# Kernel optimization log

Hardware: AMD Instinct MI355X
Metric: run time of the kernel (lower is better)

## Reference

```python
import jax, jax.numpy as jnp
import numpy as np
from jax import lax

N_SAMPLES1 = 128   # self.n_samples[0]
K = 64             # k in sample_and_group
RADIUS = 0.4       # self.radius[0]
BN_EPS = 1e-5
NEG_INF = -1e8
DIMS0 = [6, 64, 64, 128]      # mlps_in[0][0] -> mlps[0]
DIMS1 = [131, 128, 128, 512]  # 128+3 -> mlps[1] (use_light_weight=False)


def _fps(pos, n):
    # pos: (N,3) -> (n,) indices; deterministic start at point 0
    Np = pos.shape[0]
    def body(carry, _):
        dists, last = carry
        d = jnp.sum((pos - pos[last]) ** 2, axis=-1)
        dists = jnp.minimum(dists, d)
        return (dists, jnp.argmax(dists).astype(jnp.int32)), last
    _, idxs = lax.scan(body, (jnp.full((Np,), 1e10, pos.dtype), jnp.int32(0)), None, length=n)
    return idxs


def _gather(values, idx):
    # values (B,N,C), idx (B,...) -> (B,...,C)
    return jax.vmap(lambda v, i: v[i])(values, idx)


def _conv_bn_relu(x, W, b, g, be):
    # 1x1 Conv2d + BatchNorm2d (training-mode batch stats) + ReLU; x (B,n,k,Cin)
    y = jnp.einsum('bnkc,cd->bnkd', x, W) + b
    m = jnp.mean(y, axis=(0, 1, 2), keepdims=True)
    v = jnp.mean(jnp.square(y - m), axis=(0, 1, 2), keepdims=True)
    return jax.nn.relu((y - m) * lax.rsqrt(v + BN_EPS) * g + be)


def _forward(x, pos,
             W00, b00, g00, be00, W01, b01, g01, be01, W02, b02, g02, be02,
             W10, b10, g10, be10, W11, b11, g11, be11, W12, b12, g12, be12):
    # ---- stage 0: FPS + kNN grouping + conv-MLP + radius-masked max pool ----
    fidx = jax.vmap(lambda p: _fps(p, N_SAMPLES1))(pos)          # (B,128)
    sp = _gather(pos, fidx)                                      # (B,128,3) sampled_pos
    # squared pairwise distances (||a||^2+||b||^2-2ab); topk/mask on sq dist is
    # equivalent to topk/mask on sqrt dist (monotone), avoids sqrt(0) NaN grads
    sq = (jnp.sum(sp ** 2, -1)[:, :, None] + jnp.sum(pos ** 2, -1)[:, None, :]
          - 2.0 * jnp.einsum('bmd,bnd->bmn', sp, pos))           # (B,128,N)
    sq = jnp.maximum(sq, 0.0)
    neg, tidx = lax.top_k(-sq, K)                                # smallest-k
    topk_sq = -neg                                               # (B,128,64)
    gp = _gather(pos, tidx) - sp[:, :, None, :]                  # centered grouped pos
    gf = jnp.concatenate([gp, _gather(x, tidx)], axis=-1)        # (B,128,64,6)
    for (W, b, g, be) in ((W00, b00, g00, be00), (W01, b01, g01, be01), (W02, b02, g02, be02)):
        gf = _conv_bn_relu(gf, W, b, g, be)                      # (B,128,64,128)
    mask = topk_sq <= RADIUS * RADIUS
    x1 = jnp.max(jnp.where(mask[..., None], gf, NEG_INF), axis=2)  # (B,128,128)
    # ---- stage 1: global (n_samples == 1) ----
    g2 = jnp.concatenate([sp, x1], axis=-1)[:, None]             # (B,1,128,131)
    for (W, b, g, be) in ((W10, b10, g10, be10), (W11, b11, g11, be11), (W12, b12, g12, be12)):
        g2 = _conv_bn_relu(g2, W, b, g, be)                      # (B,1,128,512)
    global_x = jnp.max(g2[:, 0], axis=1, keepdims=True)          # (B,1,512)
    return global_x


def setup_inputs() -> dict:
    key = jax.random.key(0)
    ks = jax.random.split(key, 16)
    B, N = 16, 8192
    inp = {
        'x': jax.random.normal(ks[0], (B, N, 3), jnp.float32),
        'pos': jax.random.uniform(ks[1], (B, N, 3), jnp.float32),
    }
    ki = 2
    for li, dims in enumerate([DIMS0, DIMS1]):
        for ci in range(3):
            cin, cout = dims[ci], dims[ci + 1]
            inp[f'W{li}{ci}'] = jax.random.normal(ks[ki], (cin, cout), jnp.float32) * 0.05
            inp[f'b{li}{ci}'] = jnp.zeros((cout,), jnp.float32)
            inp[f'g{li}{ci}'] = jnp.ones((cout,), jnp.float32)
            inp[f'be{li}{ci}'] = jnp.zeros((cout,), jnp.float32)
            ki += 1
    return inp


def reference(x, pos,
              W00, b00, g00, be00, W01, b01, g01, be01, W02, b02, g02, be02,
              W10, b10, g10, be10, W11, b11, g11, be11, W12, b12, g12, be12):
    global_x = _forward(x, pos,
                        W00, b00, g00, be00, W01, b01, g01, be01, W02, b02, g02, be02,
                        W10, b10, g10, be10, W11, b11, g11, be11, W12, b12, g12, be12)
    pos_out = jnp.zeros((pos.shape[0], 1, 3), pos.dtype)
    return global_x, pos_out
```

## Files before the change

### kernel.cpp

```cpp
#include <hip/hip_runtime.h>
#include <cstdint>
#include <cstddef>

#define NPTS 8192
#define BATCH 16
#define MS 128
#define KNB 64
#define NBLK (BATCH * MS)

__device__ __forceinline__ float dpp_wave_max_f32(float v) {
  v = fmaxf(v, __int_as_float(__builtin_amdgcn_update_dpp((int)0xff800000, __float_as_int(v), 0x111, 0xf, 0xf, false)));
  v = fmaxf(v, __int_as_float(__builtin_amdgcn_update_dpp((int)0xff800000, __float_as_int(v), 0x112, 0xf, 0xf, false)));
  v = fmaxf(v, __int_as_float(__builtin_amdgcn_update_dpp((int)0xff800000, __float_as_int(v), 0x114, 0xf, 0xf, false)));
  v = fmaxf(v, __int_as_float(__builtin_amdgcn_update_dpp((int)0xff800000, __float_as_int(v), 0x118, 0xf, 0xf, false)));
  v = fmaxf(v, __int_as_float(__builtin_amdgcn_update_dpp((int)0xff800000, __float_as_int(v), 0x142, 0xa, 0xf, false)));
  v = fmaxf(v, __int_as_float(__builtin_amdgcn_update_dpp((int)0xff800000, __float_as_int(v), 0x143, 0xc, 0xf, false)));
  return v;
}

__device__ __forceinline__ float dpp_wave_min_f32(float v) {
  v = fminf(v, __int_as_float(__builtin_amdgcn_update_dpp(0x7f800000, __float_as_int(v), 0x111, 0xf, 0xf, false)));
  v = fminf(v, __int_as_float(__builtin_amdgcn_update_dpp(0x7f800000, __float_as_int(v), 0x112, 0xf, 0xf, false)));
  v = fminf(v, __int_as_float(__builtin_amdgcn_update_dpp(0x7f800000, __float_as_int(v), 0x114, 0xf, 0xf, false)));
  v = fminf(v, __int_as_float(__builtin_amdgcn_update_dpp(0x7f800000, __float_as_int(v), 0x118, 0xf, 0xf, false)));
  v = fminf(v, __int_as_float(__builtin_amdgcn_update_dpp(0x7f800000, __float_as_int(v), 0x142, 0xa, 0xf, false)));
  v = fminf(v, __int_as_float(__builtin_amdgcn_update_dpp(0x7f800000, __float_as_int(v), 0x143, 0xc, 0xf, false)));
  return v;
}

__device__ __forceinline__ unsigned dpp_wave_min_u32(unsigned v) {
  unsigned o;
  o = (unsigned)__builtin_amdgcn_update_dpp((int)0xffffffffu, (int)v, 0x111, 0xf, 0xf, false); v = (o < v) ? o : v;
  o = (unsigned)__builtin_amdgcn_update_dpp((int)0xffffffffu, (int)v, 0x112, 0xf, 0xf, false); v = (o < v) ? o : v;
  o = (unsigned)__builtin_amdgcn_update_dpp((int)0xffffffffu, (int)v, 0x114, 0xf, 0xf, false); v = (o < v) ? o : v;
  o = (unsigned)__builtin_amdgcn_update_dpp((int)0xffffffffu, (int)v, 0x118, 0xf, 0xf, false); v = (o < v) ? o : v;
  o = (unsigned)__builtin_amdgcn_update_dpp((int)0xffffffffu, (int)v, 0x142, 0xa, 0xf, false); v = (o < v) ? o : v;
  o = (unsigned)__builtin_amdgcn_update_dpp((int)0xffffffffu, (int)v, 0x143, 0xc, 0xf, false); v = (o < v) ? o : v;
  return v;
}

__device__ __forceinline__ float dpp_row_max_f32(float v) {
  v = fmaxf(v, __int_as_float(__builtin_amdgcn_update_dpp((int)0xff800000, __float_as_int(v), 0x111, 0xf, 0xf, false)));
  v = fmaxf(v, __int_as_float(__builtin_amdgcn_update_dpp((int)0xff800000, __float_as_int(v), 0x112, 0xf, 0xf, false)));
  v = fmaxf(v, __int_as_float(__builtin_amdgcn_update_dpp((int)0xff800000, __float_as_int(v), 0x114, 0xf, 0xf, false)));
  v = fmaxf(v, __int_as_float(__builtin_amdgcn_update_dpp((int)0xff800000, __float_as_int(v), 0x118, 0xf, 0xf, false)));
  return v;
}

__device__ __forceinline__ unsigned dpp_row_min_u32(unsigned v) {
  unsigned o;
  o = (unsigned)__builtin_amdgcn_update_dpp((int)0xffffffffu, (int)v, 0x111, 0xf, 0xf, false); v = (o < v) ? o : v;
  o = (unsigned)__builtin_amdgcn_update_dpp((int)0xffffffffu, (int)v, 0x112, 0xf, 0xf, false); v = (o < v) ? o : v;
  o = (unsigned)__builtin_amdgcn_update_dpp((int)0xffffffffu, (int)v, 0x114, 0xf, 0xf, false); v = (o < v) ? o : v;
  o = (unsigned)__builtin_amdgcn_update_dpp((int)0xffffffffu, (int)v, 0x118, 0xf, 0xf, false); v = (o < v) ? o : v;
  return v;
}

__device__ __forceinline__ float dpp_quad_min_f32(float v) {
  v = fminf(v, __int_as_float(__builtin_amdgcn_update_dpp(0x7f800000, __float_as_int(v), 0x111, 0xf, 0xf, false)));
  v = fminf(v, __int_as_float(__builtin_amdgcn_update_dpp(0x7f800000, __float_as_int(v), 0x112, 0xf, 0xf, false)));
  return v;
}

__device__ __forceinline__ unsigned dpp_quad_min_u32(unsigned v) {
  unsigned o;
  o = (unsigned)__builtin_amdgcn_update_dpp((int)0xffffffffu, (int)v, 0x111, 0xf, 0xf, false); v = (o < v) ? o : v;
  o = (unsigned)__builtin_amdgcn_update_dpp((int)0xffffffffu, (int)v, 0x112, 0xf, 0xf, false); v = (o < v) ? o : v;
  return v;
}

#define FPS_STEP(J)                                                        \
  {                                                                        \
    const float4 p = pts4[J * 1024 + t];                                   \
    const float dx = p.x - lx;                                             \
    const float dy = p.y - ly;                                             \
    const float dz = p.z - lz;                                             \
    const float d = dx * dx + dy * dy + dz * dz;                           \
    md##J = fminf(md##J, d);                                               \
  }

#define FPS_RESCAN(J)                                                      \
  if (md##J == wv) best = (unsigned)(J * 1024 + t);

__global__ __launch_bounds__(1024, 4) void fps_kernel(const float* __restrict__ pos,
                                                      float* __restrict__ sp) {
#pragma clang fp contract(off)
  extern __shared__ float4 pts4[];
  __shared__ float wval[2][16];
  __shared__ unsigned widx[2][16];
  const int b = blockIdx.x;
  const float* P = pos + (size_t)b * NPTS * 3;
  const int t = threadIdx.x;
  const int wave = t >> 6;
  const int lane = t & 63;
  float md0 = 1e10f, md1 = 1e10f, md2 = 1e10f, md3 = 1e10f;
  float md4 = 1e10f, md5 = 1e10f, md6 = 1e10f, md7 = 1e10f;
  for (int i = t; i < NPTS; i += 1024)
    pts4[i] = make_float4(P[i * 3 + 0], P[i * 3 + 1], P[i * 3 + 2], 0.f);
  float lx = P[0], ly = P[1], lz = P[2];
  __syncthreads();
  for (int it = 0; it < MS; ++it) {
    if (t == 0) {
      sp[((size_t)b * MS + it) * 3 + 0] = lx;
      sp[((size_t)b * MS + it) * 3 + 1] = ly;
      sp[((size_t)b * MS + it) * 3 + 2] = lz;
    }
    FPS_STEP(0) FPS_STEP(1) FPS_STEP(2) FPS_STEP(3)
    FPS_STEP(4) FPS_STEP(5) FPS_STEP(6) FPS_STEP(7)
    const float m01 = fmaxf(md0, md1), m23 = fmaxf(md2, md3);
    const float m45 = fmaxf(md4, md5), m67 = fmaxf(md6, md7);
    const float bv = fmaxf(fmaxf(m01, m23), fmaxf(m45, m67));
    const float wv = __int_as_float(
        __builtin_amdgcn_readlane(__float_as_int(dpp_wave_max_f32(bv)), 63));
    unsigned best = 0xffffffffu;
    if (bv == wv) {
      FPS_RESCAN(7) FPS_RESCAN(6) FPS_RESCAN(5) FPS_RESCAN(4)
      FPS_RESCAN(3) FPS_RESCAN(2) FPS_RESCAN(1) FPS_RESCAN(0)
    }
    const unsigned wi =
        (unsigned)__builtin_amdgcn_readlane((int)dpp_wave_min_u32(best), 63);
    const int par = it & 1;
    if (lane == 0) { wval[par][wave] = wv; widx[par][wave] = wi; }
    __syncthreads();
    const float a = wval[par][lane & 15];
    const float M = __int_as_float(
        __builtin_amdgcn_readlane(__float_as_int(dpp_row_max_f32(a)), 15));
    const unsigned c2 = (a == M) ? widx[par][lane & 15] : 0xffffffffu;
    const unsigned idx =
        (unsigned)__builtin_amdgcn_readlane((int)dpp_row_min_u32(c2), 15);
    const float4 c = pts4[idx];
    lx = c.x; ly = c.y; lz = c.z;
  }
}

__global__ __launch_bounds__(256) void knn_kernel(const float* __restrict__ pos,
                                                  const float* __restrict__ xf,
                                                  const float* __restrict__ sp,
                                                  float* __restrict__ gf0,
                                                  float* __restrict__ sqsel) {
#pragma clang fp contract(off)
  __shared__ float sqv[NPTS];
  __shared__ float wval[2][4];
  __shared__ unsigned widx[2][4];
  __shared__ int sel_i[KNB];
  __shared__ float sel_v[KNB];
  const int bm = blockIdx.x;
  const int b = bm >> 7;
  const float* P = pos + (size_t)b * NPTS * 3;
  const float sx = sp[bm * 3 + 0], sy = sp[bm * 3 + 1], sz = sp[bm * 3 + 2];
  const float nsp = sx * sx + sy * sy + sz * sz;
  const int t = threadIdx.x;
  const int wave = t >> 6;
  const int lane = t & 63;
  for (int j = 0; j < 32; ++j) {
    const int i = j * 256 + t;
    const float qx = P[i * 3 + 0], qy = P[i * 3 + 1], qz = P[i * 3 + 2];
    const float npos = qx * qx + qy * qy + qz * qz;
    const float dt = sx * qx + sy * qy + sz * qz;
    float sq = (nsp + npos) - 2.0f * dt;
    sq = fmaxf(sq, 0.0f);
    sqv[i] = sq;
  }
  __syncthreads();
  float cv;
  unsigned ci;
  {
    unsigned long long k0 = ~0ULL;
    for (int j = 0; j < 32; ++j) {
      const int i = j * 256 + t;
      const unsigned long long key =
          ((unsigned long long)__float_as_uint(sqv[i]) << 32) | (unsigned)i;
      if (key < k0) k0 = key;
    }
    cv = __uint_as_float((unsigned)(k0 >> 32));
    ci = (unsigned)k0;
  }
  for (int round = 0; round < KNB; ++round) {
    const float wv = __int_as_float(
        __builtin_amdgcn_readlane(__float_as_int(dpp_wave_min_f32(cv)), 63));
    const unsigned sel = (cv == wv) ? ci : 0xffffffffu;
    const unsigned wi =
        (unsigned)__builtin_amdgcn_readlane((int)dpp_wave_min_u32(sel), 63);
    const int par = round & 1;
    if (lane == 0) { wval[par][wave] = wv; widx[par][wave] = wi; }
    __syncthreads();
    const float a = wval[par][lane & 3];
    const float M = __int_as_float(
        __builtin_amdgcn_readlane(__float_as_int(dpp_quad_min_f32(a)), 3));
    const unsigned c2 = (a == M) ? widx[par][lane & 3] : 0xffffffffu;
    const unsigned idx =
        (unsigned)__builtin_amdgcn_readlane((int)dpp_quad_min_u32(c2), 3);
    const int col = (int)(idx & 255u);
    if (t == col) {
      sel_i[round] = (int)idx;
      sel_v[round] = M;
      sqv[idx] = __uint_as_float(0x7f800000u);
    }
    if (wave == (col >> 6)) {
      float v = __uint_as_float(0x7f800000u);
      unsigned ii = 0xffffffffu;
      if (lane < 32) {
        const int i = lane * 256 + col;
        v = sqv[i];
        if (i == (int)idx) v = __uint_as_float(0x7f800000u);
        ii = (unsigned)i;
      }
      const float mv = __int_as_float(
          __builtin_amdgcn_readlane(__float_as_int(dpp_wave_min_f32(v)), 63));
      const unsigned s2 = (v == mv) ? ii : 0xffffffffu;
      const unsigned mi =
          (unsigned)__builtin_amdgcn_readlane((int)dpp_wave_min_u32(s2), 63);
      if (t == col) { cv = mv; ci = mi; }
    }
  }
  __syncthreads();
  if (t < KNB) {
    const int i = sel_i[t];
    const float* X = xf + (size_t)b * NPTS * 3;
    const size_t base = ((size_t)bm * KNB + t) * 6;
    gf0[base + 0] = P[i * 3 + 0] - sx;
    gf0[base + 1] = P[i * 3 + 1] - sy;
    gf0[base + 2] = P[i * 3 + 2] - sz;
    gf0[base + 3] = X[i * 3 + 0];
    gf0[base + 4] = X[i * 3 + 1];
    gf0[base + 5] = X[i * 3 + 2];
    sqsel[(size_t)bm * KNB + t] = sel_v[t];
  }
}


__global__ __launch_bounds__(256) void l1_kernel(
    const float* __restrict__ gf0, const float* __restrict__ W0,
    const float* __restrict__ B0,
    float* __restrict__ psum, float* __restrict__ psq,
    float* __restrict__ y1pre) {
  __shared__ float in6[64 * 8];
  __shared__ float wbuf[384];
  __shared__ float out[64 * 65];
  const int blk = blockIdx.x;
  const int t = threadIdx.x;
  const float* G = gf0 + (size_t)blk * 384;
  for (int i = t; i < 384; i += 256) in6[(i / 6) * 8 + (i % 6)] = G[i];
  for (int i = t; i < 384; i += 256) wbuf[i] = W0[i];
  __syncthreads();
  const int r = t >> 2;
  const int c0 = (t & 3) * 16;
  float acc[16];
#pragma unroll
  for (int j = 0; j < 16; ++j) acc[j] = B0[c0 + j];
  for (int cin = 0; cin < 6; ++cin) {
    const float a = in6[r * 8 + cin];
#pragma unroll
    for (int j = 0; j < 16; ++j) acc[j] = fmaf(a, wbuf[cin * 64 + c0 + j], acc[j]);
  }
#pragma unroll
  for (int j = 0; j < 16; ++j) out[r * 65 + c0 + j] = acc[j];
  __syncthreads();
  if (t < 64) {
    float s = 0.f, q = 0.f;
    for (int r2 = 0; r2 < 64; ++r2) { const float v = out[r2 * 65 + t]; s += v; q += v * v; }
    psum[(size_t)t * NBLK + blk] = s;
    psq[(size_t)t * NBLK + blk] = q;
  }
  float* Y = y1pre + (size_t)blk * 4096;
  for (int i = t; i < 4096; i += 256) Y[i] = out[(i >> 6) * 65 + (i & 63)];
}

__global__ __launch_bounds__(256) void l2_kernel(
    const float* __restrict__ ypre, const float* __restrict__ sc,
    const float* __restrict__ sh, const float* __restrict__ W1,
    const float* __restrict__ B1,
    float* __restrict__ psum, float* __restrict__ psq,
    float* __restrict__ yout) {
  __shared__ float As[64 * 68];
  __shared__ float Bs[64 * 64];
  __shared__ float out[64 * 68];
  const int blk = blockIdx.x;
  const int t = threadIdx.x;
  const float* Y = ypre + (size_t)blk * 4096;
  for (int i = t; i < 4096; i += 256) {
    const int c = i & 63;
    As[(i >> 6) * 68 + c] = fmaxf(fmaf(Y[i], sc[c], sh[c]), 0.f);
  }
  for (int i = t; i < 4096; i += 256) Bs[i] = W1[i];
  __syncthreads();
  const int tr = t >> 4;
  const int tc4 = (t & 15) * 4;
  float acc[4][4];
#pragma unroll
  for (int s = 0; s < 4; ++s)
#pragma unroll
    for (int j = 0; j < 4; ++j) acc[s][j] = B1[tc4 + j];
  for (int k0 = 0; k0 < 64; k0 += 4) {
    float4 av[4];
#pragma unroll
    for (int s = 0; s < 4; ++s)
      av[s] = *reinterpret_cast<const float4*>(&As[(tr + 16 * s) * 68 + k0]);
#pragma unroll
    for (int kk = 0; kk < 4; ++kk) {
      const float4 bv = *reinterpret_cast<const float4*>(&Bs[(k0 + kk) * 64 + tc4]);
#pragma unroll
      for (int s = 0; s < 4; ++s) {
        const float a = (kk == 0) ? av[s].x : (kk == 1) ? av[s].y
                       : (kk == 2) ? av[s].z : av[s].w;
        acc[s][0] = fmaf(a, bv.x, acc[s][0]);
        acc[s][1] = fmaf(a, bv.y, acc[s][1]);
        acc[s][2] = fmaf(a, bv.z, acc[s][2]);
        acc[s][3] = fmaf(a, bv.w, acc[s][3]);
      }
    }
  }
#pragma unroll
  for (int s = 0; s < 4; ++s) {
    float4 o;
    o.x = acc[s][0]; o.y = acc[s][1]; o.z = acc[s][2]; o.w = acc[s][3];
    *reinterpret_cast<float4*>(&out[(tr + 16 * s) * 68 + tc4]) = o;
  }
  __syncthreads();
  if (t < 64) {
    float s = 0.f, q = 0.f;
    for (int r2 = 0; r2 < 64; ++r2) { const float v = out[r2 * 68 + t]; s += v; q += v * v; }
    psum[(size_t)t * NBLK + blk] = s;
    psq[(size_t)t * NBLK + blk] = q;
  }
  float* O = yout + (size_t)blk * 4096;
  for (int i = t; i < 4096; i += 256) O[i] = out[(i >> 6) * 68 + (i & 63)];
}

__global__ __launch_bounds__(256) void l3_kernel(
    const float* __restrict__ ypre, const float* __restrict__ sc,
    const float* __restrict__ sh, const float* __restrict__ W2,
    const float* __restrict__ B2,
    float* __restrict__ psum, float* __restrict__ psq,
    float* __restrict__ yout) {
  __shared__ float As[64 * 68];
  __shared__ float Bs[64 * 64];
  __shared__ float out[64 * 68];
  const int blk = blockIdx.x;
  const int t = threadIdx.x;
  const float* Y = ypre + (size_t)blk * 4096;
  for (int i = t; i < 4096; i += 256) {
    const int c = i & 63;
    As[(i >> 6) * 68 + c] = fmaxf(fmaf(Y[i], sc[c], sh[c]), 0.f);
  }
  const int tr = t >> 4;
  const int tc4 = (t & 15) * 4;
  for (int hc = 0; hc < 2; ++hc) {
    __syncthreads();
    for (int i = t; i < 4096; i += 256)
      Bs[i] = W2[(i >> 6) * 128 + hc * 64 + (i & 63)];
    __syncthreads();
    float acc[4][4];
#pragma unroll
    for (int s = 0; s < 4; ++s)
#pragma unroll
      for (int j = 0; j < 4; ++j) acc[s][j] = B2[hc * 64 + tc4 + j];
    for (int k0 = 0; k0 < 64; k0 += 4) {
      float4 av[4];
#pragma unroll
      for (int s = 0; s < 4; ++s)
        av[s] = *reinterpret_cast<const float4*>(&As[(tr + 16 * s) * 68 + k0]);
#pragma unroll
      for (int kk = 0; kk < 4; ++kk) {
        const float4 bv = *reinterpret_cast<const float4*>(&Bs[(k0 + kk) * 64 + tc4]);
#pragma unroll
        for (int s = 0; s < 4; ++s) {
          const float a = (kk == 0) ? av[s].x : (kk == 1) ? av[s].y
                         : (kk == 2) ? av[s].z : av[s].w;
          acc[s][0] = fmaf(a, bv.x, acc[s][0]);
          acc[s][1] = fmaf(a, bv.y, acc[s][1]);
          acc[s][2] = fmaf(a, bv.z, acc[s][2]);
          acc[s][3] = fmaf(a, bv.w, acc[s][3]);
        }
      }
    }
#pragma unroll
    for (int s = 0; s < 4; ++s) {
      float4 o;
      o.x = acc[s][0]; o.y = acc[s][1]; o.z = acc[s][2]; o.w = acc[s][3];
      *reinterpret_cast<float4*>(&out[(tr + 16 * s) * 68 + tc4]) = o;
    }
    __syncthreads();
    if (t < 64) {
      float s = 0.f, q = 0.f;
      for (int r2 = 0; r2 < 64; ++r2) { const float v = out[r2 * 68 + t]; s += v; q += v * v; }
      psum[(size_t)(hc * 64 + t) * NBLK + blk] = s;
      psq[(size_t)(hc * 64 + t) * NBLK + blk] = q;
    }
    float* O = yout + (size_t)blk * 8192;
    for (int i = t; i < 4096; i += 256)
      O[(i >> 6) * 128 + hc * 64 + (i & 63)] = out[(i >> 6) * 68 + (i & 63)];
  }
}

__global__ __launch_bounds__(128) void l4_kernel(
    const float* __restrict__ y3pre, const float* __restrict__ sc3,
    const float* __restrict__ sh3, const float* __restrict__ sqsel,
    float* __restrict__ x1) {
  __shared__ float sqs[64];
  const int blk = blockIdx.x;
  const int t = threadIdx.x;
  if (t < 64) sqs[t] = sqsel[(size_t)blk * 64 + t];
  __syncthreads();
  const float scv = sc3[t], shv = sh3[t];
  const float* Y = y3pre + (size_t)blk * 8192;
  float mx = -1e8f;
  for (int r = 0; r < 64; ++r) {
    const float act = fmaxf(fmaf(Y[r * 128 + t], scv, shv), 0.f);
    const float v = (sqs[r] <= 0.16f) ? act : -1e8f;
    mx = fmaxf(mx, v);
  }
  x1[(size_t)blk * 128 + t] = mx;
}

template <int MODE>
__global__ __launch_bounds__(256) void chain_kernel(
    const float* __restrict__ gf0,
    const float* __restrict__ W0, const float* __restrict__ B0,
    const float* __restrict__ W1, const float* __restrict__ B1,
    const float* __restrict__ W2, const float* __restrict__ B2,
    const float* __restrict__ sc1, const float* __restrict__ sh1,
    const float* __restrict__ sc2, const float* __restrict__ sh2,
    const float* __restrict__ sc3, const float* __restrict__ sh3,
    const float* __restrict__ sqsel,
    float* __restrict__ psum, float* __restrict__ psq, float* __restrict__ x1) {
  __shared__ float tA[64 * 65];
  __shared__ float tB[64 * 65];
  __shared__ float wbuf[64 * 64];
  __shared__ float in6[64 * 8];
  __shared__ float sqs[64];
  const int blk = blockIdx.x;
  const int t = threadIdx.x;
  {
    const float* G = gf0 + (size_t)blk * 64 * 6;
    for (int i = t; i < 384; i += 256) in6[(i / 6) * 8 + (i % 6)] = G[i];
    for (int i = t; i < 384; i += 256) wbuf[i] = W0[i];
    if (MODE == 4 && t < 64) sqs[t] = sqsel[(size_t)blk * 64 + t];
  }
  __syncthreads();
  const int r = t >> 2;
  const int c0 = (t & 3) * 16;
  float acc[16];
#pragma unroll
  for (int j = 0; j < 16; ++j) acc[j] = B0[c0 + j];
  for (int cin = 0; cin < 6; ++cin) {
    const float a = in6[r * 8 + cin];
#pragma unroll
    for (int j = 0; j < 16; ++j) acc[j] = fmaf(a, wbuf[cin * 64 + c0 + j], acc[j]);
  }
  if (MODE == 1) {
#pragma unroll
    for (int j = 0; j < 16; ++j) tA[r * 65 + c0 + j] = acc[j];
    __syncthreads();
    if (t < 64) {
      float s = 0.f, q = 0.f;
      for (int r2 = 0; r2 < 64; ++r2) { const float v = tA[r2 * 65 + t]; s += v; q += v * v; }
      psum[(size_t)t * NBLK + blk] = s;
      psq[(size_t)t * NBLK + blk] = q;
    }
    return;
  }
#pragma unroll
  for (int j = 0; j < 16; ++j) {
    const int c = c0 + j;
    tA[r * 65 + c] = fmaxf(fmaf(acc[j], sc1[c], sh1[c]), 0.f);
  }
  __syncthreads();
  for (int i = t; i < 4096; i += 256) wbuf[i] = W1[i];
  __syncthreads();
#pragma unroll
  for (int j = 0; j < 16; ++j) acc[j] = B1[c0 + j];
  for (int cin = 0; cin < 64; ++cin) {
    const float a = tA[r * 65 + cin];
    const float4* w4 = reinterpret_cast<const float4*>(&wbuf[cin * 64 + c0]);
#pragma unroll
    for (int k = 0; k < 4; ++k) {
      const float4 w = w4[k];
      acc[k * 4 + 0] = fmaf(a, w.x, acc[k * 4 + 0]);
      acc[k * 4 + 1] = fmaf(a, w.y, acc[k * 4 + 1]);
      acc[k * 4 + 2] = fmaf(a, w.z, acc[k * 4 + 2]);
      acc[k * 4 + 3] = fmaf(a, w.w, acc[k * 4 + 3]);
    }
  }
  if (MODE == 2) {
#pragma unroll
    for (int j = 0; j < 16; ++j) tB[r * 65 + c0 + j] = acc[j];
    __syncthreads();
    if (t < 64) {
      float s = 0.f, q = 0.f;
      for (int r2 = 0; r2 < 64; ++r2) { const float v = tB[r2 * 65 + t]; s += v; q += v * v; }
      psum[(size_t)t * NBLK + blk] = s;
      psq[(size_t)t * NBLK + blk] = q;
    }
    return;
  }
#pragma unroll
  for (int j = 0; j < 16; ++j) {
    const int c = c0 + j;
    tB[r * 65 + c] = fmaxf(fmaf(acc[j], sc2[c], sh2[c]), 0.f);
  }
  for (int hc = 0; hc < 2; ++hc) {
    __syncthreads();
    for (int i = t; i < 4096; i += 256) {
      const int cin = i >> 6, cc = i & 63;
      wbuf[i] = W2[cin * 128 + hc * 64 + cc];
    }
    __syncthreads();
    float st_s = 0.f, st_q = 0.f, mx = -1e8f;
    for (int rh = 0; rh < 2; ++rh) {
      const int rr = rh * 32 + (t >> 3);
      const int cc0 = (t & 7) * 8;
      float a3[8];
#pragma unroll
      for (int j = 0; j < 8; ++j) a3[j] = B2[hc * 64 + cc0 + j];
      for (int cin = 0; cin < 64; ++cin) {
        const float a = tB[rr * 65 + cin];
        const float4* w4 = reinterpret_cast<const float4*>(&wbuf[cin * 64 + cc0]);
#pragma unroll
        for (int k = 0; k < 2; ++k) {
          const float4 w = w4[k];
          a3[k * 4 + 0] = fmaf(a, w.x, a3[k * 4 + 0]);
          a3[k * 4 + 1] = fmaf(a, w.y, a3[k * 4 + 1]);
          a3[k * 4 + 2] = fmaf(a, w.z, a3[k * 4 + 2]);
          a3[k * 4 + 3] = fmaf(a, w.w, a3[k * 4 + 3]);
        }
      }
      __syncthreads();
#pragma unroll
      for (int j = 0; j < 8; ++j) tA[(t >> 3) * 65 + cc0 + j] = a3[j];
      __syncthreads();
      if (t < 64) {
        if (MODE == 3) {
          for (int q2 = 0; q2 < 32; ++q2) { const float v = tA[q2 * 65 + t]; st_s += v; st_q += v * v; }
        } else {
          const float scv = sc3[hc * 64 + t], shv = sh3[hc * 64 + t];
          for (int q2 = 0; q2 < 32; ++q2) {
            const int kidx = rh * 32 + q2;
            const float y = tA[q2 * 65 + t];
            const float act = fmaxf(fmaf(y, scv, shv), 0.f);
            const float v = (sqs[kidx] <= 0.16f) ? act : -1e8f;
            mx = fmaxf(mx, v);
          }
        }
      }
      __syncthreads();
    }
    if (t < 64) {
      if (MODE == 3) {
        psum[(size_t)(hc * 64 + t) * NBLK + blk] = st_s;
        psq[(size_t)(hc * 64 + t) * NBLK + blk] = st_q;
      } else if (MODE == 4) {
        x1[(size_t)blk * 128 + hc * 64 + t] = mx;
      }
    }
  }
}

__global__ __launch_bounds__(256) void p_stats(const float* __restrict__ psum,
                                               const float* __restrict__ psq,
                                               float invN,
                                               const float* __restrict__ g,
                                               const float* __restrict__ be,
                                               float* __restrict__ sc,
                                               float* __restrict__ sh) {
  const int c = blockIdx.x;
  const int t = threadIdx.x;
  double s = 0.0, q = 0.0;
  for (int k = t; k < NBLK; k += 256) {
    s += (double)psum[(size_t)c * NBLK + k];
    q += (double)psq[(size_t)c * NBLK + k];
  }
  __shared__ double ss[256], qq[256];
  ss[t] = s;
  qq[t] = q;
  __syncthreads();
  for (int st = 128; st > 0; st >>= 1) {
    if (t < st) { ss[t] += ss[t + st]; qq[t] += qq[t + st]; }
    __syncthreads();
  }
  if (t == 0) {
    const double mean = ss[0] * (double)invN;
    double var = qq[0] * (double)invN - mean * mean;
    if (var < 0.0) var = 0.0;
    const float scl = (float)((double)g[c] / sqrt(var + 1e-5));
    sc[c] = scl;
    sh[c] = be[c] - (float)mean * scl;
  }
}

__global__ __launch_bounds__(128) void s1_kernel(const float* __restrict__ sp,
                                                 const float* __restrict__ x1,
                                                 const float* __restrict__ W,
                                                 const float* __restrict__ bia,
                                                 float* __restrict__ y1) {
  __shared__ float row[132];
  const int rowid = blockIdx.x;
  const int t = threadIdx.x;
  if (t < 3) row[t] = sp[(size_t)rowid * 3 + t];
  row[3 + t] = x1[(size_t)rowid * 128 + t];
  __syncthreads();
  float acc = bia[t];
  for (int cin = 0; cin < 131; ++cin) acc = fmaf(row[cin], W[(size_t)cin * 128 + t], acc);
  y1[(size_t)rowid * 128 + t] = acc;
}

__global__ __launch_bounds__(128) void s2_kernel(const float* __restrict__ y1,
                                                 const float* __restrict__ sc, const float* __restrict__ sh,
                                                 const float* __restrict__ W, const float* __restrict__ bia,
                                                 float* __restrict__ y2) {
  __shared__ float row[128];
  const int rowid = blockIdx.x;
  const int t = threadIdx.x;
  row[t] = fmaxf(fmaf(y1[(size_t)rowid * 128 + t], sc[t], sh[t]), 0.f);
  __syncthreads();
  float acc = bia[t];
  for (int cin = 0; cin < 128; ++cin) acc = fmaf(row[cin], W[(size_t)cin * 128 + t], acc);
  y2[(size_t)rowid * 128 + t] = acc;
}

__global__ __launch_bounds__(256) void s3_kernel(const float* __restrict__ y2,
                                                 const float* __restrict__ sc, const float* __restrict__ sh,
                                                 const float* __restrict__ W, const float* __restrict__ bia,
                                                 float* __restrict__ y3) {
  __shared__ float row[128];
  const int rowid = blockIdx.x;
  const int t = threadIdx.x;
  if (t < 128) row[t] = fmaxf(fmaf(y2[(size_t)rowid * 128 + t], sc[t], sh[t]), 0.f);
  __syncthreads();
  for (int h = 0; h < 2; ++h) {
    const int c = h * 256 + t;
    float acc = bia[c];
    for (int cin = 0; cin < 128; ++cin) acc = fmaf(row[cin], W[(size_t)cin * 512 + c], acc);
    y3[(size_t)rowid * 512 + c] = acc;
  }
}

__global__ __launch_bounds__(256) void s_stats(const float* __restrict__ y, int C, int rows,
                                               const float* __restrict__ g, const float* __restrict__ be,
                                               float* __restrict__ sc, float* __restrict__ sh) {
  const int c = blockIdx.x;
  const int t = threadIdx.x;
  double s = 0.0, q = 0.0;
  for (int r2 = t; r2 < rows; r2 += 256) {
    const double v = (double)y[(size_t)r2 * C + c];
    s += v;
    q += v * v;
  }
  __shared__ double ss[256], qq[256];
  ss[t] = s;
  qq[t] = q;
  __syncthreads();
  for (int st = 128; st > 0; st >>= 1) {
    if (t < st) { ss[t] += ss[t + st]; qq[t] += qq[t + st]; }
    __syncthreads();
  }
  if (t == 0) {
    const double mean = ss[0] / rows;
    double var = qq[0] / rows - mean * mean;
    if (var < 0.0) var = 0.0;
    const float scl = (float)((double)g[c] / sqrt(var + 1e-5));
    sc[c] = scl;
    sh[c] = be[c] - (float)mean * scl;
  }
}

__global__ __launch_bounds__(256) void final_kernel(const float* __restrict__ y3,
                                                    const float* __restrict__ sc, const float* __restrict__ sh,
                                                    float* __restrict__ out) {
  const int gid = blockIdx.x * 256 + threadIdx.x;
  const int b = gid >> 9;
  const int c = gid & 511;
  const float scv = sc[c], shv = sh[c];
  float mx = -3.402823466e+38f;
  for (int m = 0; m < 128; ++m) {
    const float v = fmaxf(fmaf(y3[((size_t)(b * 128 + m)) * 512 + c], scv, shv), 0.f);
    mx = fmaxf(mx, v);
  }
  out[gid] = mx;
  if (gid < 48) out[8192 + gid] = 0.f;
}

extern "C" void kernel_launch(void* const* d_in, const int* in_sizes, int n_in,
                              void* d_out, int out_size, void* d_ws, size_t ws_size,
                              hipStream_t stream) {
  const float* x    = (const float*)d_in[0];
  const float* pos  = (const float*)d_in[1];
  const float* W00  = (const float*)d_in[2];
  const float* b00  = (const float*)d_in[3];
  const float* g00  = (const float*)d_in[4];
  const float* be00 = (const float*)d_in[5];
  const float* W01  = (const float*)d_in[6];
  const float* b01  = (const float*)d_in[7];
  const float* g01  = (const float*)d_in[8];
  const float* be01 = (const float*)d_in[9];
  const float* W02  = (const float*)d_in[10];
  const float* b02  = (const float*)d_in[11];
  const float* g02  = (const float*)d_in[12];
  const float* be02 = (const float*)d_in[13];
  const float* W10  = (const float*)d_in[14];
  const float* b10  = (const float*)d_in[15];
  const float* g10  = (const float*)d_in[16];
  const float* be10 = (const float*)d_in[17];
  const float* W11  = (const float*)d_in[18];
  const float* b11  = (const float*)d_in[19];
  const float* g11  = (const float*)d_in[20];
  const float* be11 = (const float*)d_in[21];
  const float* W12  = (const float*)d_in[22];
  const float* b12  = (const float*)d_in[23];
  const float* g12  = (const float*)d_in[24];
  const float* be12 = (const float*)d_in[25];

  float* w = (float*)d_ws;
  float* sp    = w;
  float* gf0   = sp + 6144;
  float* sqsel = gf0 + 786432;
  float* x1    = sqsel + 131072;
  float* parts = x1 + 262144;
  float* psum  = parts;
  float* psq   = parts + 128 * NBLK;
  float* st    = parts + 524288;
  float* sc1 = st + 0,    *sh1 = st + 64;
  float* sc2 = st + 128,  *sh2 = st + 192;
  float* sc3 = st + 256,  *sh3 = st + 384;
  float* t1sc = st + 512, *t1sh = st + 640;
  float* t2sc = st + 768, *t2sh = st + 896;
  float* t3sc = st + 1024, *t3sh = st + 1536;
  float* y1s = st + 2048;
  float* y2s = y1s + 262144;
  float* y3s = y2s + 262144;
  const size_t BASE = 3284992;
  float* y1pre = w + BASE;
  float* y2pre = y1pre + 8388608;
  float* y3pre = y2pre + 8388608;
  const size_t NEED = BASE + 8388608ULL * 2 + 16777216ULL;
  const bool big = ws_size >= NEED * sizeof(float);

  fps_kernel<<<BATCH, 1024, NPTS * sizeof(float4), stream>>>(pos, sp);
  knn_kernel<<<BATCH * MS, 256, 0, stream>>>(pos, x, sp, gf0, sqsel);

  const float invN0 = 1.0f / (float)(NBLK * KNB);
  if (big) {
    l1_kernel<<<NBLK, 256, 0, stream>>>(gf0, W00, b00, psum, psq, y1pre);
    p_stats<<<64, 256, 0, stream>>>(psum, psq, invN0, g00, be00, sc1, sh1);
    l2_kernel<<<NBLK, 256, 0, stream>>>(y1pre, sc1, sh1, W01, b01, psum, psq, y2pre);
    p_stats<<<64, 256, 0, stream>>>(psum, psq, invN0, g01, be01, sc2, sh2);
    l3_kernel<<<NBLK, 256, 0, stream>>>(y2pre, sc2, sh2, W02, b02, psum, psq, y3pre);
    p_stats<<<128, 256, 0, stream>>>(psum, psq, invN0, g02, be02, sc3, sh3);
    l4_kernel<<<NBLK, 128, 0, stream>>>(y3pre, sc3, sh3, sqsel, x1);
  } else {
    chain_kernel<1><<<NBLK, 256, 0, stream>>>(gf0, W00, b00, W01, b01, W02, b02,
                                              sc1, sh1, sc2, sh2, sc3, sh3, sqsel, psum, psq, x1);
    p_stats<<<64, 256, 0, stream>>>(psum, psq, invN0, g00, be00, sc1, sh1);
    chain_kernel<2><<<NBLK, 256, 0, stream>>>(gf0, W00, b00, W01, b01, W02, b02,
                                              sc1, sh1, sc2, sh2, sc3, sh3, sqsel, psum, psq, x1);
    p_stats<<<64, 256, 0, stream>>>(psum, psq, invN0, g01, be01, sc2, sh2);
    chain_kernel<3><<<NBLK, 256, 0, stream>>>(gf0, W00, b00, W01, b01, W02, b02,
                                              sc1, sh1, sc2, sh2, sc3, sh3, sqsel, psum, psq, x1);
    p_stats<<<128, 256, 0, stream>>>(psum, psq, invN0, g02, be02, sc3, sh3);
    chain_kernel<4><<<NBLK, 256, 0, stream>>>(gf0, W00, b00, W01, b01, W02, b02,
                                              sc1, sh1, sc2, sh2, sc3, sh3, sqsel, psum, psq, x1);
  }

  s1_kernel<<<NBLK, 128, 0, stream>>>(sp, x1, W10, b10, y1s);
  s_stats<<<128, 256, 0, stream>>>(y1s, 128, NBLK, g10, be10, t1sc, t1sh);
  s2_kernel<<<NBLK, 128, 0, stream>>>(y1s, t1sc, t1sh, W11, b11, y2s);
  s_stats<<<128, 256, 0, stream>>>(y2s, 128, NBLK, g11, be11, t2sc, t2sh);
  s3_kernel<<<NBLK, 256, 0, stream>>>(y2s, t2sc, t2sh, W12, b12, y3s);
  s_stats<<<512, 256, 0, stream>>>(y3s, 512, NBLK, g12, be12, t3sc, t3sh);
  final_kernel<<<32, 256, 0, stream>>>(y3s, t3sc, t3sh, (float*)d_out);
}
```

Measured before the change: 440.5 us.

## Make kNN top-k selection per-wave without block barriers, then merge lists

The kNN kernel now has each of its four waves pick its own 64 smallest candidates without a block-wide barrier per round. It tracks already-taken entries with a per-column bitmask rather than writing infinity into shared memory, and pads the shared distance array to avoid bank conflicts. The four sorted per-wave lists are then merged by binary-search ranking to get the global top 64. Distance computation is fused into the initial min scan, and the unused chain_kernel fallback is removed so the big-workspace path is always taken. This risks failing if the workspace is smaller than required.

After: 432.2 us. No clear change (-1.9%).

```diff
diff --git a/kernel.cpp b/kernel.cpp
--- a/kernel.cpp
+++ b/kernel.cpp
@@ -53,19 +53,6 @@
   o = (unsigned)__builtin_amdgcn_update_dpp((int)0xffffffffu, (int)v, 0x112, 0xf, 0xf, false); v = (o < v) ? o : v;
   o = (unsigned)__builtin_amdgcn_update_dpp((int)0xffffffffu, (int)v, 0x114, 0xf, 0xf, false); v = (o < v) ? o : v;
   o = (unsigned)__builtin_amdgcn_update_dpp((int)0xffffffffu, (int)v, 0x118, 0xf, 0xf, false); v = (o < v) ? o : v;
-  return v;
-}
-
-__device__ __forceinline__ float dpp_quad_min_f32(float v) {
-  v = fminf(v, __int_as_float(__builtin_amdgcn_update_dpp(0x7f800000, __float_as_int(v), 0x111, 0xf, 0xf, false)));
-  v = fminf(v, __int_as_float(__builtin_amdgcn_update_dpp(0x7f800000, __float_as_int(v), 0x112, 0xf, 0xf, false)));
-  return v;
-}
-
-__device__ __forceinline__ unsigned dpp_quad_min_u32(unsigned v) {
-  unsigned o;
-  o = (unsigned)__builtin_amdgcn_update_dpp((int)0xffffffffu, (int)v, 0x111, 0xf, 0xf, false); v = (o < v) ? o : v;
-  o = (unsigned)__builtin_amdgcn_update_dpp((int)0xffffffffu, (int)v, 0x112, 0xf, 0xf, false); v = (o < v) ? o : v;
   return v;
 }
 
@@ -139,11 +126,9 @@
                                                   float* __restrict__ gf0,
                                                   float* __restrict__ sqsel) {
 #pragma clang fp contract(off)
-  __shared__ float sqv[NPTS];
-  __shared__ float wval[2][4];
-  __shared__ unsigned widx[2][4];
-  __shared__ int sel_i[KNB];
-  __shared__ float sel_v[KNB];
+  __shared__ float sqv[NPTS + 32];
+  __shared__ unsigned long long wlist[4][KNB];
+  __shared__ unsigned long long selk[KNB];
   const int bm = blockIdx.x;
   const int b = bm >> 7;
   const float* P = pos + (size_t)b * NPTS * 3;
@@ -152,70 +137,76 @@
   const int t = threadIdx.x;
   const int wave = t >> 6;
   const int lane = t & 63;
-  for (int j = 0; j < 32; ++j) {
-    const int i = j * 256 + t;
-    const float qx = P[i * 3 + 0], qy = P[i * 3 + 1], qz = P[i * 3 + 2];
-    const float npos = qx * qx + qy * qy + qz * qz;
-    const float dt = sx * qx + sy * qy + sz * qz;
-    float sq = (nsp + npos) - 2.0f * dt;
-    sq = fmaxf(sq, 0.0f);
-    sqv[i] = sq;
-  }
-  __syncthreads();
   float cv;
   unsigned ci;
   {
     unsigned long long k0 = ~0ULL;
     for (int j = 0; j < 32; ++j) {
       const int i = j * 256 + t;
+      const float qx = P[i * 3 + 0], qy = P[i * 3 + 1], qz = P[i * 3 + 2];
+      const float npos = qx * qx + qy * qy + qz * qz;
+      const float dt = sx * qx + sy * qy + sz * qz;
+      float sq = (nsp + npos) - 2.0f * dt;
+      sq = fmaxf(sq, 0.0f);
+      sqv[i + j] = sq;
       const unsigned long long key =
-          ((unsigned long long)__float_as_uint(sqv[i]) << 32) | (unsigned)i;
+          ((unsigned long long)__float_as_uint(sq) << 32) | (unsigned)i;
       if (key < k0) k0 = key;
     }
     cv = __uint_as_float((unsigned)(k0 >> 32));
     ci = (unsigned)k0;
   }
+  __syncthreads();
+  unsigned cmask = 0u;
   for (int round = 0; round < KNB; ++round) {
     const float wv = __int_as_float(
         __builtin_amdgcn_readlane(__float_as_int(dpp_wave_min_f32(cv)), 63));
     const unsigned sel = (cv == wv) ? ci : 0xffffffffu;
     const unsigned wi =
         (unsigned)__builtin_amdgcn_readlane((int)dpp_wave_min_u32(sel), 63);
-    const int par = round & 1;
-    if (lane == 0) { wval[par][wave] = wv; widx[par][wave] = wi; }
-    __syncthreads();
-    const float a = wval[par][lane & 3];
-    const float M = __int_as_float(
-        __builtin_amdgcn_readlane(__float_as_int(dpp_quad_min_f32(a)), 3));
-    const unsigned c2 = (a == M) ? widx[par][lane & 3] : 0xffffffffu;
-    const unsigned idx =
-        (unsigned)__builtin_amdgcn_readlane((int)dpp_quad_min_u32(c2), 3);
-    const int col = (int)(idx & 255u);
-    if (t == col) {
-      sel_i[round] = (int)idx;
-      sel_v[round] = M;
-      sqv[idx] = __uint_as_float(0x7f800000u);
-    }
-    if (wave == (col >> 6)) {
-      float v = __uint_as_float(0x7f800000u);
-      unsigned ii = 0xffffffffu;
-      if (lane < 32) {
-        const int i = lane * 256 + col;
-        v = sqv[i];
-        if (i == (int)idx) v = __uint_as_float(0x7f800000u);
-        ii = (unsigned)i;
-      }
-      const float mv = __int_as_float(
-          __builtin_amdgcn_readlane(__float_as_int(dpp_wave_min_f32(v)), 63));
-      const unsigned s2 = (v == mv) ? ii : 0xffffffffu;
-      const unsigned mi =
-          (unsigned)__builtin_amdgcn_readlane((int)dpp_wave_min_u32(s2), 63);
-      if (t == col) { cv = mv; ci = mi; }
-    }
+    if (lane == 0)
+      wlist[wave][round] =
+          ((unsigned long long)__float_as_uint(wv) << 32) | wi;
+    const int col = (int)(wi & 255u);
+    const int ownerLane = col & 63;
+    const unsigned jsel = wi >> 8;
+    if (lane == ownerLane) cmask |= (1u << jsel);
+    const unsigned omask =
+        (unsigned)__builtin_amdgcn_readlane((int)cmask, ownerLane);
+    float v = __uint_as_float(0x7f800000u);
+    unsigned ii = 0xffffffffu;
+    if (lane < 32 && !((omask >> lane) & 1u)) {
+      const int i = lane * 256 + col;
+      v = sqv[i + lane];
+      ii = (unsigned)i;
+    }
+    const float mv = __int_as_float(
+        __builtin_amdgcn_readlane(__float_as_int(dpp_wave_min_f32(v)), 63));
+    const unsigned s2 = (v == mv) ? ii : 0xffffffffu;
+    const unsigned mi =
+        (unsigned)__builtin_amdgcn_readlane((int)dpp_wave_min_u32(s2), 63);
+    if (lane == ownerLane) { cv = mv; ci = mi; }
+  }
+  __syncthreads();
+  {
+    const int w = wave, r = lane;
+    const unsigned long long e = wlist[w][r];
+    int rank = r;
+#pragma unroll
+    for (int w2 = 0; w2 < 4; ++w2) {
+      if (w2 == w) continue;
+      int lo = 0;
+#pragma unroll
+      for (int step = 32; step > 0; step >>= 1)
+        if (lo + step <= KNB && wlist[w2][lo + step - 1] < e) lo += step;
+      rank += lo;
+    }
+    if (rank < KNB) selk[rank] = e;
   }
   __syncthreads();
   if (t < KNB) {
-    const int i = sel_i[t];
+    const unsigned long long e = selk[t];
+    const int i = (int)(e & 0xffffffffu);
     const float* X = xf + (size_t)b * NPTS * 3;
     const size_t base = ((size_t)bm * KNB + t) * 6;
     gf0[base + 0] = P[i * 3 + 0] - sx;
@@ -224,7 +215,7 @@
     gf0[base + 3] = X[i * 3 + 0];
     gf0[base + 4] = X[i * 3 + 1];
     gf0[base + 5] = X[i * 3 + 2];
-    sqsel[(size_t)bm * KNB + t] = sel_v[t];
+    sqsel[(size_t)bm * KNB + t] = __uint_as_float((unsigned)(e >> 32));
   }
 }
 
@@ -411,149 +402,6 @@
     mx = fmaxf(mx, v);
   }
   x1[(size_t)blk * 128 + t] = mx;
-}
-
-template <int MODE>
-__global__ __launch_bounds__(256) void chain_kernel(
-    const float* __restrict__ gf0,
-    const float* __restrict__ W0, const float* __restrict__ B0,
-    const float* __restrict__ W1, const float* __restrict__ B1,
-    const float* __restrict__ W2, const float* __restrict__ B2,
-    const float* __restrict__ sc1, const float* __restrict__ sh1,
-    const float* __restrict__ sc2, const float* __restrict__ sh2,
-    const float* __restrict__ sc3, const float* __restrict__ sh3,
-    const float* __restrict__ sqsel,
-    float* __restrict__ psum, float* __restrict__ psq, float* __restrict__ x1) {
-  __shared__ float tA[64 * 65];
-  __shared__ float tB[64 * 65];
-  __shared__ float wbuf[64 * 64];
-  __shared__ float in6[64 * 8];
-  __shared__ float sqs[64];
-  const int blk = blockIdx.x;
-  const int t = threadIdx.x;
-  {
-    const float* G = gf0 + (size_t)blk * 64 * 6;
-    for (int i = t; i < 384; i += 256) in6[(i / 6) * 8 + (i % 6)] = G[i];
-    for (int i = t; i < 384; i += 256) wbuf[i] = W0[i];
-    if (MODE == 4 && t < 64) sqs[t] = sqsel[(size_t)blk * 64 + t];
-  }
-  __syncthreads();
-  const int r = t >> 2;
-  const int c0 = (t & 3) * 16;
-  float acc[16];
-#pragma unroll
-  for (int j = 0; j < 16; ++j) acc[j] = B0[c0 + j];
-  for (int cin = 0; cin < 6; ++cin) {
-    const float a = in6[r * 8 + cin];
-#pragma unroll
-    for (int j = 0; j < 16; ++j) acc[j] = fmaf(a, wbuf[cin * 64 + c0 + j], acc[j]);
-  }
-  if (MODE == 1) {
-#pragma unroll
-    for (int j = 0; j < 16; ++j) tA[r * 65 + c0 + j] = acc[j];
-    __syncthreads();
-    if (t < 64) {
-      float s = 0.f, q = 0.f;
-      for (int r2 = 0; r2 < 64; ++r2) { const float v = tA[r2 * 65 + t]; s += v; q += v * v; }
-      psum[(size_t)t * NBLK + blk] = s;
-      psq[(size_t)t * NBLK + blk] = q;
-    }
-    return;
-  }
-#pragma unroll
-  for (int j = 0; j < 16; ++j) {
-    const int c = c0 + j;
-    tA[r * 65 + c] = fmaxf(fmaf(acc[j], sc1[c], sh1[c]), 0.f);
-  }
-  __syncthreads();
-  for (int i = t; i < 4096; i += 256) wbuf[i] = W1[i];
-  __syncthreads();
-#pragma unroll
-  for (int j = 0; j < 16; ++j) acc[j] = B1[c0 + j];
-  for (int cin = 0; cin < 64; ++cin) {
-    const float a = tA[r * 65 + cin];
-    const float4* w4 = reinterpret_cast<const float4*>(&wbuf[cin * 64 + c0]);
-#pragma unroll
-    for (int k = 0; k < 4; ++k) {
-      const float4 w = w4[k];
-      acc[k * 4 + 0] = fmaf(a, w.x, acc[k * 4 + 0]);
-      acc[k * 4 + 1] = fmaf(a, w.y, acc[k * 4 + 1]);
-      acc[k * 4 + 2] = fmaf(a, w.z, acc[k * 4 + 2]);
-      acc[k * 4 + 3] = fmaf(a, w.w, acc[k * 4 + 3]);
-    }
-  }
-  if (MODE == 2) {
-#pragma unroll
-    for (int j = 0; j < 16; ++j) tB[r * 65 + c0 + j] = acc[j];
-    __syncthreads();
-    if (t < 64) {
-      float s = 0.f, q = 0.f;
-      for (int r2 = 0; r2 < 64; ++r2) { const float v = tB[r2 * 65 + t]; s += v; q += v * v; }
-      psum[(size_t)t * NBLK + blk] = s;
-      psq[(size_t)t * NBLK + blk] = q;
-    }
-    return;
-  }
-#pragma unroll
-  for (int j = 0; j < 16; ++j) {
-    const int c = c0 + j;
-    tB[r * 65 + c] = fmaxf(fmaf(acc[j], sc2[c], sh2[c]), 0.f);
-  }
-  for (int hc = 0; hc < 2; ++hc) {
-    __syncthreads();
-    for (int i = t; i < 4096; i += 256) {
-      const int cin = i >> 6, cc = i & 63;
-      wbuf[i] = W2[cin * 128 + hc * 64 + cc];
-    }
-    __syncthreads();
-    float st_s = 0.f, st_q = 0.f, mx = -1e8f;
-    for (int rh = 0; rh < 2; ++rh) {
-      const int rr = rh * 32 + (t >> 3);
-      const int cc0 = (t & 7) * 8;
-      float a3[8];
-#pragma unroll
-      for (int j = 0; j < 8; ++j) a3[j] = B2[hc * 64 + cc0 + j];
-      for (int cin = 0; cin < 64; ++cin) {
-        const float a = tB[rr * 65 + cin];
-        const float4* w4 = reinterpret_cast<const float4*>(&wbuf[cin * 64 + cc0]);
-#pragma unroll
-        for (int k = 0; k < 2; ++k) {
-          const float4 w = w4[k];
-          a3[k * 4 + 0] = fmaf(a, w.x, a3[k * 4 + 0]);
-          a3[k * 4 + 1] = fmaf(a, w.y, a3[k * 4 + 1]);
-          a3[k * 4 + 2] = fmaf(a, w.z, a3[k * 4 + 2]);
-          a3[k * 4 + 3] = fmaf(a, w.w, a3[k * 4 + 3]);
-        }
-      }
-      __syncthreads();
-#pragma unroll
-      for (int j = 0; j < 8; ++j) tA[(t >> 3) * 65 + cc0 + j] = a3[j];
-      __syncthreads();
-      if (t < 64) {
-        if (MODE == 3) {
-          for (int q2 = 0; q2 < 32; ++q2) { const float v = tA[q2 * 65 + t]; st_s += v; st_q += v * v; }
-        } else {
-          const float scv = sc3[hc * 64 + t], shv = sh3[hc * 64 + t];
-          for (int q2 = 0; q2 < 32; ++q2) {
-            const int kidx = rh * 32 + q2;
-            const float y = tA[q2 * 65 + t];
-            const float act = fmaxf(fmaf(y, scv, shv), 0.f);
-            const float v = (sqs[kidx] <= 0.16f) ? act : -1e8f;
-            mx = fmaxf(mx, v);
-          }
-        }
-      }
-      __syncthreads();
-    }
-    if (t < 64) {
-      if (MODE == 3) {
-        psum[(size_t)(hc * 64 + t) * NBLK + blk] = st_s;
-        psq[(size_t)(hc * 64 + t) * NBLK + blk] = st_q;
-      } else if (MODE == 4) {
-        x1[(size_t)blk * 128 + hc * 64 + t] = mx;
-      }
-    }
-  }
 }
 
 __global__ __launch_bounds__(256) void p_stats(const float* __restrict__ psum,
@@ -733,33 +581,19 @@
   float* y2pre = y1pre + 8388608;
   float* y3pre = y2pre + 8388608;
   const size_t NEED = BASE + 8388608ULL * 2 + 16777216ULL;
-  const bool big = ws_size >= NEED * sizeof(float);
+  (void)NEED;
 
   fps_kernel<<<BATCH, 1024, NPTS * sizeof(float4), stream>>>(pos, sp);
   knn_kernel<<<BATCH * MS, 256, 0, stream>>>(pos, x, sp, gf0, sqsel);
 
   const float invN0 = 1.0f / (float)(NBLK * KNB);
-  if (big) {
-    l1_kernel<<<NBLK, 256, 0, stream>>>(gf0, W00, b00, psum, psq, y1pre);
-    p_stats<<<64, 256, 0, stream>>>(psum, psq, invN0, g00, be00, sc1, sh1);
-    l2_kernel<<<NBLK, 256, 0, stream>>>(y1pre, sc1, sh1, W01, b01, psum, psq, y2pre);
-    p_stats<<<64, 256, 0, stream>>>(psum, psq, invN0, g01, be01, sc2, sh2);
-    l3_kernel<<<NBLK, 256, 0, stream>>>(y2pre, sc2, sh2, W02, b02, psum, psq, y3pre);
-    p_stats<<<128, 256, 0, stream>>>(psum, psq, invN0, g02, be02, sc3, sh3);
-    l4_kernel<<<NBLK, 128, 0, stream>>>(y3pre, sc3, sh3, sqsel, x1);
-  } else {
-    chain_kernel<1><<<NBLK, 256, 0, stream>>>(gf0, W00, b00, W01, b01, W02, b02,
-                                              sc1, sh1, sc2, sh2, sc3, sh3, sqsel, psum, psq, x1);
-    p_stats<<<64, 256, 0, stream>>>(psum, psq, invN0, g00, be00, sc1, sh1);
-    chain_kernel<2><<<NBLK, 256, 0, stream>>>(gf0, W00, b00, W01, b01, W02, b02,
-                                              sc1, sh1, sc2, sh2, sc3, sh3, sqsel, psum, psq, x1);
-    p_stats<<<64, 256, 0, stream>>>(psum, psq, invN0, g01, be01, sc2, sh2);
-    chain_kernel<3><<<NBLK, 256, 0, stream>>>(gf0, W00, b00, W01, b01, W02, b02,
-                                              sc1, sh1, sc2, sh2, sc3, sh3, sqsel, psum, psq, x1);
-    p_stats<<<128, 256, 0, stream>>>(psum, psq, invN0, g02, be02, sc3, sh3);
-    chain_kernel<4><<<NBLK, 256, 0, stream>>>(gf0, W00, b00, W01, b01, W02, b02,
-                                              sc1, sh1, sc2, sh2, sc3, sh3, sqsel, psum, psq, x1);
-  }
+  l1_kernel<<<NBLK, 256, 0, stream>>>(gf0, W00, b00, psum, psq, y1pre);
+  p_stats<<<64, 256, 0, stream>>>(psum, psq, invN0, g00, be00, sc1, sh1);
+  l2_kernel<<<NBLK, 256, 0, stream>>>(y1pre, sc1, sh1, W01, b01, psum, psq, y2pre);
+  p_stats<<<64, 256, 0, stream>>>(psum, psq, invN0, g01, be01, sc2, sh2);
+  l3_kernel<<<NBLK, 256, 0, stream>>>(y2pre, sc2, sh2, W02, b02, psum, psq, y3pre);
+  p_stats<<<128, 256, 0, stream>>>(psum, psq, invN0, g02, be02, sc3, sh3);
+  l4_kernel<<<NBLK, 128, 0, stream>>>(y3pre, sc3, sh3, sqsel, x1);
 
   s1_kernel<<<NBLK, 128, 0, stream>>>(sp, x1, W10, b10, y1s);
   s_stats<<<128, 256, 0, stream>>>(y1s, 128, NBLK, g10, be10, t1sc, t1sh);
```
